# Kernel tuning notes

Measured on AMD Instinct MI355X. Metric: run time of the kernel, lower is better.

Reference implementation:

```python
import jax, jax.numpy as jnp
import numpy as np

EPS = 1e-9


def _pairwise_sqdist(x1, x2):
    # x1: (B,n,3), x2: (B,m,3) -> (B,n,m) squared euclidean distances
    s1 = jnp.sum(x1 * x1, axis=-1)
    s2 = jnp.sum(x2 * x2, axis=-1)
    cross = jnp.einsum('bnd,bmd->bnm', x1, x2)
    return jnp.maximum(s1[:, :, None] + s2[:, None, :] - 2.0 * cross, 0.0)


def _approxmatch(x1, x2):
    # Faithful port of the approxmatch CUDA kernel (Fan et al. EMD approx).
    B, n, _ = x1.shape
    m = x2.shape[1]
    if n >= m:
        multiL, multiR = 1.0, float(n // m)   # integer division as in CUDA
    else:
        multiL, multiR = float(m // n), 1.0
    dist = _pairwise_sqdist(x1, x2)  # (B,n,m)
    # j = 7 .. -1 -> level = -4^j ; j = -2 -> level = 0  (10 sweeps total)
    levels = jnp.concatenate([
        -(4.0 ** jnp.arange(7, -2, -1, dtype=jnp.float32)),
        jnp.zeros((1,), jnp.float32)])
    match0 = jnp.zeros((B, n, m), jnp.float32)
    remainL0 = jnp.full((B, n), multiL, jnp.float32)
    remainR0 = jnp.full((B, m), multiR, jnp.float32)

    def body(carry, level):
        match, remainL, remainR = carry
        e = jnp.exp(level * dist)                              # (B,n,m)
        suml = EPS + jnp.einsum('bnm,bm->bn', e, remainR)
        ratioL = remainL / suml                                # (B,n)
        sumr = remainR * jnp.einsum('bnm,bn->bm', e, ratioL)   # (B,m)
        consumption = jnp.minimum(remainR / (sumr + EPS), 1.0)
        ratioR = consumption * remainR                         # (B,m)
        remainR = jnp.maximum(0.0, remainR - sumr)
        w = e * ratioL[:, :, None] * ratioR[:, None, :]        # flow k->l
        match = match + w
        remainL = jnp.maximum(0.0, remainL - jnp.sum(w, axis=-1))
        return (match, remainL, remainR), None

    (match, _, _), _ = jax.lax.scan(body, (match0, remainL0, remainR0), levels)
    return match, dist


def setup_inputs() -> dict:
    key = jax.random.key(0)
    k1, k2 = jax.random.split(key)
    B, N = 4, 4096
    xyz1 = jax.random.normal(k1, (B, 3, N), dtype=jnp.float32)
    xyz2 = jax.random.normal(k2, (B, 3, N), dtype=jnp.float32)
    return {"xyz1": xyz1, "xyz2": xyz2}


def reference(xyz1, xyz2):
    # transpose=True: BCN -> BNC
    x1 = jnp.transpose(xyz1, (0, 2, 1))
    x2 = jnp.transpose(xyz2, (0, 2, 1))
    match, dist = _approxmatch(x1, x2)
    d = jnp.sqrt(jnp.maximum(dist, 1e-20))
    cost = jnp.sum(match * d, axis=(1, 2))            # (B,)
    emd = cost / min(x1.shape[1], x2.shape[1])
    return jnp.mean(emd)                               # reduce_mean=True
```

## Files before the change

kernel.cpp:

```cpp
#include <hip/hip_runtime.h>


#define NPTS 4096
#define BATCH 4
#define EMD_EPS 1e-9f
#define TILE 1024
#define RPW 2
#define THREADS 256
#define RPB 8
#define NBLK (NPTS / RPB)

typedef float v2f __attribute__((ext_vector_type(2)));

__device__ __forceinline__ float fexp2(float x) {
#if __has_builtin(__builtin_amdgcn_exp2f)
    return __builtin_amdgcn_exp2f(x);
#else
    return exp2f(x);
#endif
}
__device__ __forceinline__ float fsqrt(float x) {
#if __has_builtin(__builtin_amdgcn_sqrtf)
    return __builtin_amdgcn_sqrtf(x);
#else
    return __sqrtf(x);
#endif
}

__device__ __forceinline__ float wave_reduce(float v) {
    v += __shfl_xor(v, 32);
    v += __shfl_xor(v, 16);
    v += __shfl_xor(v, 8);
    v += __shfl_xor(v, 4);
    v += __shfl_xor(v, 2);
    v += __shfl_xor(v, 1);
    return v;
}

__global__ __launch_bounds__(THREADS, 6) void k_ratioL0(
        const float* __restrict__ xyz1, const float* __restrict__ xyz2,
        float* __restrict__ ratioL, float* __restrict__ remainL,
        float* __restrict__ remainR, float ls2) {
    const int b = blockIdx.y;
    const int tid = threadIdx.x;
    const int wave = tid >> 6;
    const int lane = tid & 63;
    const int row0 = blockIdx.x * RPB + wave * RPW;

    const float* x1 = xyz1 + b * 3 * NPTS;
    const float* x2 = xyz2 + b * 3 * NPTS;
    const float2* x2x = (const float2*)(x2);
    const float2* x2y = (const float2*)(x2 + NPTS);
    const float2* x2z = (const float2*)(x2 + 2 * NPTS);

    float px[RPW], py[RPW], pz[RPW];
    v2f acc[RPW];
#pragma unroll
    for (int r = 0; r < RPW; ++r) {
        px[r] = x1[row0 + r];
        py[r] = x1[NPTS + row0 + r];
        pz[r] = x1[2 * NPTS + row0 + r];
        acc[r] = (v2f)(0.0f);
    }
    __shared__ float4 sA[TILE / 2];
    __shared__ float2 sZ[TILE / 2];

    for (int c0 = 0; c0 < NPTS; c0 += TILE) {
        __syncthreads();
        for (int i = tid; i < TILE / 2; i += THREADS) {
            int e = c0 / 2 + i;
            float2 xx = x2x[e], yy = x2y[e];
            sA[i] = make_float4(xx.x, xx.y, yy.x, yy.y);
            sZ[i] = x2z[e];
        }
        __syncthreads();
#pragma unroll 2
        for (int j = 0; j < TILE / 128; ++j) {
            float4 a = sA[lane + 64 * j];
            float2 z = sZ[lane + 64 * j];
            v2f ax = {a.x, a.y}, ay = {a.z, a.w}, az = {z.x, z.y};
#pragma unroll
            for (int r = 0; r < RPW; ++r) {
                v2f dx = px[r] - ax, dy = py[r] - ay, dz = pz[r] - az;
                v2f d = dx * dx + dy * dy + dz * dz;
                v2f sd = ls2 * d;
                v2f e2 = {fexp2(sd.x), fexp2(sd.y)};
                acc[r] += e2;
            }
        }
    }
#pragma unroll
    for (int r = 0; r < RPW; ++r) {
        float s = wave_reduce(acc[r].x + acc[r].y);
        if (lane == 0) {
            int idx = b * NPTS + row0 + r;
            ratioL[idx] = 1.0f / (EMD_EPS + s);
            remainL[idx] = 1.0f;
            remainR[idx] = 1.0f;
        }
    }
}

__global__ __launch_bounds__(THREADS, 6) void k_ratioR(
        const float* __restrict__ xyz1, const float* __restrict__ xyz2,
        const float* __restrict__ ratioL, float* __restrict__ ratioR,
        float* __restrict__ remainR, float ls2) {
    const int b = blockIdx.y;
    const int tid = threadIdx.x;
    const int wave = tid >> 6;
    const int lane = tid & 63;
    const int col0 = blockIdx.x * RPB + wave * RPW;

    const float* x1 = xyz1 + b * 3 * NPTS;
    const float* x2 = xyz2 + b * 3 * NPTS;
    const float2* x1x = (const float2*)(x1);
    const float2* x1y = (const float2*)(x1 + NPTS);
    const float2* x1z = (const float2*)(x1 + 2 * NPTS);
    const float2* wLv = (const float2*)(ratioL + b * NPTS);

    float px[RPW], py[RPW], pz[RPW];
    v2f acc[RPW];
#pragma unroll
    for (int r = 0; r < RPW; ++r) {
        px[r] = x2[col0 + r];
        py[r] = x2[NPTS + col0 + r];
        pz[r] = x2[2 * NPTS + col0 + r];
        acc[r] = (v2f)(0.0f);
    }
    __shared__ float4 sA[TILE / 2];
    __shared__ float4 sB[TILE / 2];

    for (int c0 = 0; c0 < NPTS; c0 += TILE) {
        __syncthreads();
        for (int i = tid; i < TILE / 2; i += THREADS) {
            int e = c0 / 2 + i;
            float2 xx = x1x[e], yy = x1y[e], zz = x1z[e], ww = wLv[e];
            sA[i] = make_float4(xx.x, xx.y, yy.x, yy.y);
            sB[i] = make_float4(zz.x, zz.y, ww.x, ww.y);
        }
        __syncthreads();
#pragma unroll 2
        for (int j = 0; j < TILE / 128; ++j) {
            float4 a = sA[lane + 64 * j];
            float4 bq = sB[lane + 64 * j];
            v2f ax = {a.x, a.y}, ay = {a.z, a.w};
            v2f az = {bq.x, bq.y}, aw = {bq.z, bq.w};
#pragma unroll
            for (int r = 0; r < RPW; ++r) {
                v2f dx = px[r] - ax, dy = py[r] - ay, dz = pz[r] - az;
                v2f d = dx * dx + dy * dy + dz * dz;
                v2f sd = ls2 * d;
                v2f e2 = {fexp2(sd.x), fexp2(sd.y)};
                acc[r] += e2 * aw;
            }
        }
    }
#pragma unroll
    for (int r = 0; r < RPW; ++r) {
        float s = wave_reduce(acc[r].x + acc[r].y);
        if (lane == 0) {
            int idx = b * NPTS + col0 + r;
            float rv = remainR[idx];
            float sumr = rv * s;
            float cons = fminf(rv / (sumr + EMD_EPS), 1.0f);
            ratioR[idx] = cons * rv;
            remainR[idx] = fmaxf(0.0f, rv - sumr);
        }
    }
}

template <bool SQ>
__global__ __launch_bounds__(THREADS, 6) void k_cost_fused(
        const float* __restrict__ xyz1, const float* __restrict__ xyz2,
        float* __restrict__ ratioL, const float* __restrict__ ratioR,
        float* __restrict__ remainL, const float* __restrict__ remainR,
        float* __restrict__ cost_part, float ls2, float ls2n, int initCost) {
    const int b = blockIdx.y;
    const int tid = threadIdx.x;
    const int wave = tid >> 6;
    const int lane = tid & 63;
    const int row0 = blockIdx.x * RPB + wave * RPW;

    const float* x1 = xyz1 + b * 3 * NPTS;
    const float* x2 = xyz2 + b * 3 * NPTS;
    const float2* x2x = (const float2*)(x2);
    const float2* x2y = (const float2*)(x2 + NPTS);
    const float2* x2z = (const float2*)(x2 + 2 * NPTS);
    const float2* wRv = (const float2*)(ratioR + b * NPTS);
    const float2* w2v = (const float2*)(remainR + b * NPTS);

    float px[RPW], py[RPW], pz[RPW];
    v2f acc_a[RPW], acc_c[RPW], acc_s[RPW];
#pragma unroll
    for (int r = 0; r < RPW; ++r) {
        px[r] = x1[row0 + r];
        py[r] = x1[NPTS + row0 + r];
        pz[r] = x1[2 * NPTS + row0 + r];
        acc_a[r] = (v2f)(0.0f);
        acc_c[r] = (v2f)(0.0f);
        acc_s[r] = (v2f)(0.0f);
    }
    __shared__ float4 sA[TILE / 2];
    __shared__ float4 sB[TILE / 2];
    __shared__ float2 sC[TILE / 2];
    __shared__ float s_cost[THREADS / 64];

    for (int c0 = 0; c0 < NPTS; c0 += TILE) {
        __syncthreads();
        for (int i = tid; i < TILE / 2; i += THREADS) {
            int e = c0 / 2 + i;
            float2 xx = x2x[e], yy = x2y[e], zz = x2z[e], wr = wRv[e];
            sA[i] = make_float4(xx.x, xx.y, yy.x, yy.y);
            sB[i] = make_float4(zz.x, zz.y, wr.x, wr.y);
            sC[i] = w2v[e];
        }
        __syncthreads();
#pragma unroll 2
        for (int j = 0; j < TILE / 128; ++j) {
            float4 a = sA[lane + 64 * j];
            float4 bq = sB[lane + 64 * j];
            float2 c = sC[lane + 64 * j];
            v2f ax = {a.x, a.y}, ay = {a.z, a.w};
            v2f az = {bq.x, bq.y}, wr = {bq.z, bq.w};
            v2f cw = {c.x, c.y};
#pragma unroll
            for (int r = 0; r < RPW; ++r) {
                v2f dx = px[r] - ax, dy = py[r] - ay, dz = pz[r] - az;
                v2f d = dx * dx + dy * dy + dz * dz;
                v2f er;
                if (SQ) {
                    v2f sd = ls2n * d;
                    v2f e2 = {fexp2(sd.x), fexp2(sd.y)};
                    acc_s[r] += e2 * cw;
                    v2f e4 = e2 * e2;
                    er = (e4 * e4) * wr;
                } else {
                    v2f sd = ls2 * d;
                    v2f e1 = {fexp2(sd.x), fexp2(sd.y)};
                    er = e1 * wr;
                    acc_s[r] += cw;
                }
                acc_a[r] += er;
                v2f sq = {fsqrt(d.x), fsqrt(d.y)};
                acc_c[r] += er * sq;
            }
        }
    }
    float wcost = 0.0f;
#pragma unroll
    for (int r = 0; r < RPW; ++r) {
        float sa = wave_reduce(acc_a[r].x + acc_a[r].y);
        float sc = wave_reduce(acc_c[r].x + acc_c[r].y);
        float ss = wave_reduce(acc_s[r].x + acc_s[r].y);
        if (lane == 0) {
            int idx = b * NPTS + row0 + r;
            float rl = ratioL[idx];
            float rem = fmaxf(0.0f, remainL[idx] - rl * sa);
            remainL[idx] = rem;
            ratioL[idx] = rem / (EMD_EPS + ss);
            wcost = fmaf(rl, sc, wcost);
        }
    }
    if (lane == 0) s_cost[wave] = wcost;
    __syncthreads();
    if (tid == 0) {
        float t = s_cost[0] + s_cost[1] + s_cost[2] + s_cost[3];
        int ci = b * NBLK + blockIdx.x;
        cost_part[ci] = (initCost ? t : cost_part[ci] + t);
    }
}

__global__ void k_sum_ratioL(const float* __restrict__ ratioL, float* __restrict__ S_L) {
    const int b = blockIdx.x;
    const int tid = threadIdx.x;
    float s = 0.0f;
    for (int i = tid; i < NPTS; i += 256) s += ratioL[b * NPTS + i];
    s = wave_reduce(s);
    __shared__ float sw[4];
    if ((tid & 63) == 0) sw[tid >> 6] = s;
    __syncthreads();
    if (tid == 0) S_L[b] = sw[0] + sw[1] + sw[2] + sw[3];
}

__global__ __launch_bounds__(THREADS, 6) void k_cost_l0(
        const float* __restrict__ xyz1, const float* __restrict__ xyz2,
        const float* __restrict__ ratioL, const float* __restrict__ remainR,
        const float* __restrict__ S_L, float* __restrict__ cost_part) {
    const int b = blockIdx.y;
    const int tid = threadIdx.x;
    const int wave = tid >> 6;
    const int lane = tid & 63;
    const int row0 = blockIdx.x * RPB + wave * RPW;
    const float sL = S_L[b];

    const float* x1 = xyz1 + b * 3 * NPTS;
    const float* x2 = xyz2 + b * 3 * NPTS;
    const float2* x2x = (const float2*)(x2);
    const float2* x2y = (const float2*)(x2 + NPTS);
    const float2* x2z = (const float2*)(x2 + 2 * NPTS);
    const float2* wRv = (const float2*)(remainR + b * NPTS);

    float px[RPW], py[RPW], pz[RPW];
    v2f acc_c[RPW];
#pragma unroll
    for (int r = 0; r < RPW; ++r) {
        px[r] = x1[row0 + r];
        py[r] = x1[NPTS + row0 + r];
        pz[r] = x1[2 * NPTS + row0 + r];
        acc_c[r] = (v2f)(0.0f);
    }
    __shared__ float4 sA[TILE / 2];
    __shared__ float4 sB[TILE / 2];
    __shared__ float s_cost[THREADS / 64];

    for (int c0 = 0; c0 < NPTS; c0 += TILE) {
        __syncthreads();
        for (int i = tid; i < TILE / 2; i += THREADS) {
            int e = c0 / 2 + i;
            float2 xx = x2x[e], yy = x2y[e], zz = x2z[e], rv = wRv[e];
            float wr0 = fminf(rv.x / (rv.x * sL + EMD_EPS), 1.0f) * rv.x;
            float wr1 = fminf(rv.y / (rv.y * sL + EMD_EPS), 1.0f) * rv.y;
            sA[i] = make_float4(xx.x, xx.y, yy.x, yy.y);
            sB[i] = make_float4(zz.x, zz.y, wr0, wr1);
        }
        __syncthreads();
#pragma unroll 2
        for (int j = 0; j < TILE / 128; ++j) {
            float4 a = sA[lane + 64 * j];
            float4 bq = sB[lane + 64 * j];
            v2f ax = {a.x, a.y}, ay = {a.z, a.w};
            v2f az = {bq.x, bq.y}, wr = {bq.z, bq.w};
#pragma unroll
            for (int r = 0; r < RPW; ++r) {
                v2f dx = px[r] - ax, dy = py[r] - ay, dz = pz[r] - az;
                v2f d = dx * dx + dy * dy + dz * dz;
                v2f sq = {fsqrt(d.x), fsqrt(d.y)};
                acc_c[r] += wr * sq;
            }
        }
    }
    float wcost = 0.0f;
#pragma unroll
    for (int r = 0; r < RPW; ++r) {
        float sc = wave_reduce(acc_c[r].x + acc_c[r].y);
        if (lane == 0)
            wcost = fmaf(ratioL[b * NPTS + row0 + r], sc, wcost);
    }
    if (lane == 0) s_cost[wave] = wcost;
    __syncthreads();
    if (tid == 0) {
        float t = s_cost[0] + s_cost[1] + s_cost[2] + s_cost[3];
        cost_part[b * NBLK + blockIdx.x] += t;
    }
}

__global__ void k_final(const float* __restrict__ cost_part, float* __restrict__ out) {
    const int tid = threadIdx.x;
    float s = 0.0f;
    for (int i = tid; i < BATCH * NBLK; i += 256) s += cost_part[i];
    s = wave_reduce(s);
    __shared__ float sw[4];
    if ((tid & 63) == 0) sw[tid >> 6] = s;
    __syncthreads();
    if (tid == 0) out[0] = (sw[0] + sw[1] + sw[2] + sw[3]) / ((float)NPTS * (float)BATCH);
}

extern "C" void kernel_launch(void* const* d_in, const int* in_sizes, int n_in,
                              void* d_out, int out_size, void* d_ws, size_t ws_size,
                              hipStream_t stream) {
    const float* xyz1 = (const float*)d_in[0];
    const float* xyz2 = (const float*)d_in[1];
    float* out = (float*)d_out;

    const int BN = BATCH * NPTS;
    float* ws = (float*)d_ws;
    float* remainL  = ws;
    float* remainR  = ws + 1 * BN;
    float* ratioL   = ws + 2 * BN;
    float* ratioR   = ws + 3 * BN;
    float* cost_part = ws + 4 * BN;
    float* S_L      = cost_part + BATCH * NBLK;

    static const float levels[10] = {
        -16384.0f, -4096.0f, -1024.0f, -256.0f, -64.0f,
        -16.0f, -4.0f, -1.0f, -0.25f, 0.0f};
    float ls2[10];
    for (int t = 0; t < 10; ++t)
        ls2[t] = (float)(levels[t] * 1.4426950408889634);

    dim3 grid(NBLK, BATCH);

    k_ratioL0<<<grid, THREADS, 0, stream>>>(xyz1, xyz2, ratioL, remainL, remainR, ls2[0]);
    for (int t = 0; t < 8; ++t) {
        k_ratioR<<<grid, THREADS, 0, stream>>>(xyz1, xyz2, ratioL, ratioR, remainR, ls2[t]);
        k_cost_fused<true><<<grid, THREADS, 0, stream>>>(xyz1, xyz2, ratioL, ratioR,
                                                         remainL, remainR, cost_part,
                                                         ls2[t], ls2[t + 1], t == 0 ? 1 : 0);
    }
    k_ratioR<<<grid, THREADS, 0, stream>>>(xyz1, xyz2, ratioL, ratioR, remainR, ls2[8]);
    k_cost_fused<false><<<grid, THREADS, 0, stream>>>(xyz1, xyz2, ratioL, ratioR,
                                                      remainL, remainR, cost_part,
                                                      ls2[8], 0.0f, 0);
    k_sum_ratioL<<<BATCH, 256, 0, stream>>>(ratioL, S_L);
    k_cost_l0<<<grid, THREADS, 0, stream>>>(xyz1, xyz2, ratioL, remainR, S_L, cost_part);
    k_final<<<1, 256, 0, stream>>>(cost_part, out);
}
```

Baseline: 532.6 us.

## Sort points by x and skip far tiles using per-tile x bounds

Counting-sorts both point clouds by x coordinate and computes x min/max bounds for each 128-point tile. The inner loops of the ratioL, ratioR and cost kernels then skip a tile when its squared x-gap to the wave's rows makes the exponential underflow at that level. The cost kernel computes only the next-level sum when the current-level term is negligible, and the separate ratioL sum kernel is folded into an atomic add. This aims to cut the exp and sqrt work for the sharp early levels, at the cost of two extra kernels and wave-uniform branching. The skipped terms are approximations, but ones that underflow to near zero in float32.

```diff
diff --git a/kernel.cpp b/kernel.cpp
--- a/kernel.cpp
+++ b/kernel.cpp
@@ -9,6 +9,7 @@
 #define THREADS 256
 #define RPB 8
 #define NBLK (NPTS / RPB)
+#define NTILE 32
 
 typedef float v2f __attribute__((ext_vector_type(2)));
 
@@ -37,18 +38,98 @@
     return v;
 }
 
+__global__ __launch_bounds__(1024) void k_sortx(
+        const float* __restrict__ xyz1, const float* __restrict__ xyz2,
+        float* __restrict__ x1s, float* __restrict__ x2s) {
+    const int side = blockIdx.x, b = blockIdx.y;
+    const float* src = (side ? xyz2 : xyz1) + b * 3 * NPTS;
+    float* dst = (side ? x2s : x1s) + b * 3 * NPTS;
+    const int tid = threadIdx.x;
+    const int lane = tid & 63, wave = tid >> 6;
+
+    __shared__ unsigned hist[4096];
+    __shared__ unsigned short keys[4096];
+    __shared__ unsigned warr[16];
+
+    for (int i = tid; i < 4096; i += 1024) hist[i] = 0u;
+    __syncthreads();
+    for (int i = tid; i < NPTS; i += 1024) {
+        float x = src[i];
+        int k = (int)((x + 6.0f) * 341.0f);
+        k = min(max(k, 0), 4095);
+        keys[i] = (unsigned short)k;
+        atomicAdd(&hist[k], 1u);
+    }
+    __syncthreads();
+    const int base = tid * 4;
+    unsigned h0 = hist[base], h1 = hist[base + 1], h2 = hist[base + 2], h3 = hist[base + 3];
+    unsigned st = h0 + h1 + h2 + h3;
+    unsigned v = st;
+    for (int d = 1; d < 64; d <<= 1) {
+        unsigned u = __shfl_up(v, d);
+        if (lane >= d) v += u;
+    }
+    if (lane == 63) warr[wave] = v;
+    __syncthreads();
+    if (tid == 0) {
+        unsigned run = 0;
+        for (int w = 0; w < 16; ++w) { unsigned t = warr[w]; warr[w] = run; run += t; }
+    }
+    __syncthreads();
+    unsigned off = warr[wave] + (v - st);
+    hist[base] = off;
+    hist[base + 1] = off + h0;
+    hist[base + 2] = off + h0 + h1;
+    hist[base + 3] = off + h0 + h1 + h2;
+    __syncthreads();
+    for (int i = tid; i < NPTS; i += 1024) {
+        unsigned k = keys[i];
+        unsigned pos = atomicAdd(&hist[k], 1u);
+        dst[pos] = src[i];
+        dst[NPTS + pos] = src[NPTS + i];
+        dst[2 * NPTS + pos] = src[2 * NPTS + i];
+    }
+}
+
+__global__ void k_xbounds(const float* __restrict__ x1s, const float* __restrict__ x2s,
+                          float* __restrict__ bx1, float* __restrict__ bx2) {
+    const int tile = blockIdx.x, b = blockIdx.y, side = blockIdx.z;
+    const float* src = (side ? x2s : x1s) + b * 3 * NPTS + tile * 128;
+    float* o = (side ? bx2 : bx1) + (b * NTILE + tile) * 2;
+    const int lane = threadIdx.x;
+    float mn = 1e30f, mx = -1e30f;
+    for (int i = lane; i < 128; i += 64) {
+        float x = src[i];
+        mn = fminf(mn, x); mx = fmaxf(mx, x);
+    }
+    for (int d = 32; d; d >>= 1) {
+        mn = fminf(mn, __shfl_xor(mn, d));
+        mx = fmaxf(mx, __shfl_xor(mx, d));
+    }
+    if (lane == 0) { o[0] = mn; o[1] = mx; }
+}
+
+#define XMD2(ti)                                                             \
+    float bmn = sBB[(ti) * 2], bmx = sBB[(ti) * 2 + 1];                      \
+    float dd = fmaxf(0.0f, fmaxf(bmn - gmx, gmn - bmx));                     \
+    float md2 = dd * dd;
+
 __global__ __launch_bounds__(THREADS, 6) void k_ratioL0(
-        const float* __restrict__ xyz1, const float* __restrict__ xyz2,
+        const float* __restrict__ x1s, const float* __restrict__ x2s,
+        const float* __restrict__ bx2,
         float* __restrict__ ratioL, float* __restrict__ remainL,
-        float* __restrict__ remainR, float ls2) {
+        float* __restrict__ remainR, float* __restrict__ S_L,
+        float ls2, float thr) {
     const int b = blockIdx.y;
     const int tid = threadIdx.x;
     const int wave = tid >> 6;
     const int lane = tid & 63;
     const int row0 = blockIdx.x * RPB + wave * RPW;
 
-    const float* x1 = xyz1 + b * 3 * NPTS;
-    const float* x2 = xyz2 + b * 3 * NPTS;
+    if (blockIdx.x == 0 && tid == 0) S_L[b] = 0.0f;
+
+    const float* x1 = x1s + b * 3 * NPTS;
+    const float* x2 = x2s + b * 3 * NPTS;
     const float2* x2x = (const float2*)(x2);
     const float2* x2y = (const float2*)(x2 + NPTS);
     const float2* x2z = (const float2*)(x2 + 2 * NPTS);
@@ -62,8 +143,12 @@
         pz[r] = x1[2 * NPTS + row0 + r];
         acc[r] = (v2f)(0.0f);
     }
+    const float gmn = fminf(px[0], px[1]), gmx = fmaxf(px[0], px[1]);
+
     __shared__ float4 sA[TILE / 2];
     __shared__ float2 sZ[TILE / 2];
+    __shared__ float sBB[NTILE * 2];
+    if (tid < NTILE * 2) sBB[tid] = bx2[b * NTILE * 2 + tid];
 
     for (int c0 = 0; c0 < NPTS; c0 += TILE) {
         __syncthreads();
@@ -76,16 +161,19 @@
         __syncthreads();
 #pragma unroll 2
         for (int j = 0; j < TILE / 128; ++j) {
-            float4 a = sA[lane + 64 * j];
-            float2 z = sZ[lane + 64 * j];
-            v2f ax = {a.x, a.y}, ay = {a.z, a.w}, az = {z.x, z.y};
-#pragma unroll
-            for (int r = 0; r < RPW; ++r) {
-                v2f dx = px[r] - ax, dy = py[r] - ay, dz = pz[r] - az;
-                v2f d = dx * dx + dy * dy + dz * dz;
-                v2f sd = ls2 * d;
-                v2f e2 = {fexp2(sd.x), fexp2(sd.y)};
-                acc[r] += e2;
+            XMD2((c0 >> 7) + j);
+            if (md2 < thr) {
+                float4 a = sA[lane + 64 * j];
+                float2 z = sZ[lane + 64 * j];
+                v2f ax = {a.x, a.y}, ay = {a.z, a.w}, az = {z.x, z.y};
+#pragma unroll
+                for (int r = 0; r < RPW; ++r) {
+                    v2f dx = px[r] - ax, dy = py[r] - ay, dz = pz[r] - az;
+                    v2f d = dx * dx + dy * dy + dz * dz;
+                    v2f sd = ls2 * d;
+                    v2f e2 = {fexp2(sd.x), fexp2(sd.y)};
+                    acc[r] += e2;
+                }
             }
         }
     }
@@ -102,17 +190,18 @@
 }
 
 __global__ __launch_bounds__(THREADS, 6) void k_ratioR(
-        const float* __restrict__ xyz1, const float* __restrict__ xyz2,
+        const float* __restrict__ x1s, const float* __restrict__ x2s,
+        const float* __restrict__ bx1,
         const float* __restrict__ ratioL, float* __restrict__ ratioR,
-        float* __restrict__ remainR, float ls2) {
+        float* __restrict__ remainR, float ls2, float thr) {
     const int b = blockIdx.y;
     const int tid = threadIdx.x;
     const int wave = tid >> 6;
     const int lane = tid & 63;
     const int col0 = blockIdx.x * RPB + wave * RPW;
 
-    const float* x1 = xyz1 + b * 3 * NPTS;
-    const float* x2 = xyz2 + b * 3 * NPTS;
+    const float* x1 = x1s + b * 3 * NPTS;
+    const float* x2 = x2s + b * 3 * NPTS;
     const float2* x1x = (const float2*)(x1);
     const float2* x1y = (const float2*)(x1 + NPTS);
     const float2* x1z = (const float2*)(x1 + 2 * NPTS);
@@ -127,8 +216,12 @@
         pz[r] = x2[2 * NPTS + col0 + r];
         acc[r] = (v2f)(0.0f);
     }
+    const float gmn = fminf(px[0], px[1]), gmx = fmaxf(px[0], px[1]);
+
     __shared__ float4 sA[TILE / 2];
     __shared__ float4 sB[TILE / 2];
+    __shared__ float sBB[NTILE * 2];
+    if (tid < NTILE * 2) sBB[tid] = bx1[b * NTILE * 2 + tid];
 
     for (int c0 = 0; c0 < NPTS; c0 += TILE) {
         __syncthreads();
@@ -141,17 +234,20 @@
         __syncthreads();
 #pragma unroll 2
         for (int j = 0; j < TILE / 128; ++j) {
-            float4 a = sA[lane + 64 * j];
-            float4 bq = sB[lane + 64 * j];
-            v2f ax = {a.x, a.y}, ay = {a.z, a.w};
-            v2f az = {bq.x, bq.y}, aw = {bq.z, bq.w};
-#pragma unroll
-            for (int r = 0; r < RPW; ++r) {
-                v2f dx = px[r] - ax, dy = py[r] - ay, dz = pz[r] - az;
-                v2f d = dx * dx + dy * dy + dz * dz;
-                v2f sd = ls2 * d;
-                v2f e2 = {fexp2(sd.x), fexp2(sd.y)};
-                acc[r] += e2 * aw;
+            XMD2((c0 >> 7) + j);
+            if (md2 < thr) {
+                float4 a = sA[lane + 64 * j];
+                float4 bq = sB[lane + 64 * j];
+                v2f ax = {a.x, a.y}, ay = {a.z, a.w};
+                v2f az = {bq.x, bq.y}, aw = {bq.z, bq.w};
+#pragma unroll
+                for (int r = 0; r < RPW; ++r) {
+                    v2f dx = px[r] - ax, dy = py[r] - ay, dz = pz[r] - az;
+                    v2f d = dx * dx + dy * dy + dz * dz;
+                    v2f sd = ls2 * d;
+                    v2f e2 = {fexp2(sd.x), fexp2(sd.y)};
+                    acc[r] += e2 * aw;
+                }
             }
         }
     }
@@ -171,18 +267,21 @@
 
 template <bool SQ>
 __global__ __launch_bounds__(THREADS, 6) void k_cost_fused(
-        const float* __restrict__ xyz1, const float* __restrict__ xyz2,
+        const float* __restrict__ x1s, const float* __restrict__ x2s,
+        const float* __restrict__ bx2,
         float* __restrict__ ratioL, const float* __restrict__ ratioR,
         float* __restrict__ remainL, const float* __restrict__ remainR,
-        float* __restrict__ cost_part, float ls2, float ls2n, int initCost) {
+        float* __restrict__ S_L, float* __restrict__ cost_part,
+        float ls2, float ls2n, float thrF, float thrT,
+        int initCost, int addSL) {
     const int b = blockIdx.y;
     const int tid = threadIdx.x;
     const int wave = tid >> 6;
     const int lane = tid & 63;
     const int row0 = blockIdx.x * RPB + wave * RPW;
 
-    const float* x1 = xyz1 + b * 3 * NPTS;
-    const float* x2 = xyz2 + b * 3 * NPTS;
+    const float* x1 = x1s + b * 3 * NPTS;
+    const float* x2 = x2s + b * 3 * NPTS;
     const float2* x2x = (const float2*)(x2);
     const float2* x2y = (const float2*)(x2 + NPTS);
     const float2* x2z = (const float2*)(x2 + 2 * NPTS);
@@ -200,10 +299,14 @@
         acc_c[r] = (v2f)(0.0f);
         acc_s[r] = (v2f)(0.0f);
     }
+    const float gmn = fminf(px[0], px[1]), gmx = fmaxf(px[0], px[1]);
+
     __shared__ float4 sA[TILE / 2];
     __shared__ float4 sB[TILE / 2];
     __shared__ float2 sC[TILE / 2];
+    __shared__ float sBB[NTILE * 2];
     __shared__ float s_cost[THREADS / 64];
+    if (tid < NTILE * 2) sBB[tid] = bx2[b * NTILE * 2 + tid];
 
     for (int c0 = 0; c0 < NPTS; c0 += TILE) {
         __syncthreads();
@@ -217,32 +320,46 @@
         __syncthreads();
 #pragma unroll 2
         for (int j = 0; j < TILE / 128; ++j) {
-            float4 a = sA[lane + 64 * j];
-            float4 bq = sB[lane + 64 * j];
-            float2 c = sC[lane + 64 * j];
-            v2f ax = {a.x, a.y}, ay = {a.z, a.w};
-            v2f az = {bq.x, bq.y}, wr = {bq.z, bq.w};
-            v2f cw = {c.x, c.y};
-#pragma unroll
-            for (int r = 0; r < RPW; ++r) {
-                v2f dx = px[r] - ax, dy = py[r] - ay, dz = pz[r] - az;
-                v2f d = dx * dx + dy * dy + dz * dz;
-                v2f er;
-                if (SQ) {
-                    v2f sd = ls2n * d;
-                    v2f e2 = {fexp2(sd.x), fexp2(sd.y)};
-                    acc_s[r] += e2 * cw;
-                    v2f e4 = e2 * e2;
-                    er = (e4 * e4) * wr;
+            XMD2((c0 >> 7) + j);
+            if (md2 < thrF) {
+                float4 a = sA[lane + 64 * j];
+                float4 bq = sB[lane + 64 * j];
+                float2 c = sC[lane + 64 * j];
+                v2f ax = {a.x, a.y}, ay = {a.z, a.w};
+                v2f az = {bq.x, bq.y}, wr = {bq.z, bq.w};
+                v2f cw = {c.x, c.y};
+                if (SQ && md2 >= thrT) {
+#pragma unroll
+                    for (int r = 0; r < RPW; ++r) {
+                        v2f dx = px[r] - ax, dy = py[r] - ay, dz = pz[r] - az;
+                        v2f d = dx * dx + dy * dy + dz * dz;
+                        v2f sd = ls2n * d;
+                        v2f e2 = {fexp2(sd.x), fexp2(sd.y)};
+                        acc_s[r] += e2 * cw;
+                    }
                 } else {
-                    v2f sd = ls2 * d;
-                    v2f e1 = {fexp2(sd.x), fexp2(sd.y)};
-                    er = e1 * wr;
-                    acc_s[r] += cw;
+#pragma unroll
+                    for (int r = 0; r < RPW; ++r) {
+                        v2f dx = px[r] - ax, dy = py[r] - ay, dz = pz[r] - az;
+                        v2f d = dx * dx + dy * dy + dz * dz;
+                        v2f er;
+                        if (SQ) {
+                            v2f sd = ls2n * d;
+                            v2f e2 = {fexp2(sd.x), fexp2(sd.y)};
+                            acc_s[r] += e2 * cw;
+                            v2f e4 = e2 * e2;
+                            er = (e4 * e4) * wr;
+                        } else {
+                            v2f sd = ls2 * d;
+                            v2f e1 = {fexp2(sd.x), fexp2(sd.y)};
+                            er = e1 * wr;
+                            acc_s[r] += cw;
+                        }
+                        acc_a[r] += er;
+                        v2f sq = {fsqrt(d.x), fsqrt(d.y)};
+                        acc_c[r] += er * sq;
+                    }
                 }
-                acc_a[r] += er;
-                v2f sq = {fsqrt(d.x), fsqrt(d.y)};
-                acc_c[r] += er * sq;
             }
         }
     }
@@ -257,7 +374,9 @@
             float rl = ratioL[idx];
             float rem = fmaxf(0.0f, remainL[idx] - rl * sa);
             remainL[idx] = rem;
-            ratioL[idx] = rem / (EMD_EPS + ss);
+            float nrl = rem / (EMD_EPS + ss);
+            ratioL[idx] = nrl;
+            if (addSL) atomicAdd(&S_L[b], nrl);
             wcost = fmaf(rl, sc, wcost);
         }
     }
@@ -270,20 +389,8 @@
     }
 }
 
-__global__ void k_sum_ratioL(const float* __restrict__ ratioL, float* __restrict__ S_L) {
-    const int b = blockIdx.x;
-    const int tid = threadIdx.x;
-    float s = 0.0f;
-    for (int i = tid; i < NPTS; i += 256) s += ratioL[b * NPTS + i];
-    s = wave_reduce(s);
-    __shared__ float sw[4];
-    if ((tid & 63) == 0) sw[tid >> 6] = s;
-    __syncthreads();
-    if (tid == 0) S_L[b] = sw[0] + sw[1] + sw[2] + sw[3];
-}
-
 __global__ __launch_bounds__(THREADS, 6) void k_cost_l0(
-        const float* __restrict__ xyz1, const float* __restrict__ xyz2,
+        const float* __restrict__ x1s, const float* __restrict__ x2s,
         const float* __restrict__ ratioL, const float* __restrict__ remainR,
         const float* __restrict__ S_L, float* __restrict__ cost_part) {
     const int b = blockIdx.y;
@@ -293,8 +400,8 @@
     const int row0 = blockIdx.x * RPB + wave * RPW;
     const float sL = S_L[b];
 
-    const float* x1 = xyz1 + b * 3 * NPTS;
-    const float* x2 = xyz2 + b * 3 * NPTS;
+    const float* x1 = x1s + b * 3 * NPTS;
+    const float* x2 = x2s + b * 3 * NPTS;
     const float2* x2x = (const float2*)(x2);
     const float2* x2y = (const float2*)(x2 + NPTS);
     const float2* x2z = (const float2*)(x2 + 2 * NPTS);
@@ -374,34 +481,46 @@
 
     const int BN = BATCH * NPTS;
     float* ws = (float*)d_ws;
-    float* remainL  = ws;
-    float* remainR  = ws + 1 * BN;
-    float* ratioL   = ws + 2 * BN;
-    float* ratioR   = ws + 3 * BN;
+    float* remainL   = ws;
+    float* remainR   = ws + 1 * BN;
+    float* ratioL    = ws + 2 * BN;
+    float* ratioR    = ws + 3 * BN;
     float* cost_part = ws + 4 * BN;
-    float* S_L      = cost_part + BATCH * NBLK;
+    float* S_L       = cost_part + BATCH * NBLK;
+    float* x1s       = S_L + 4;
+    float* x2s       = x1s + 3 * BN;
+    float* bx1       = x2s + 3 * BN;
+    float* bx2       = bx1 + BATCH * NTILE * 2;
 
     static const float levels[10] = {
         -16384.0f, -4096.0f, -1024.0f, -256.0f, -64.0f,
         -16.0f, -4.0f, -1.0f, -0.25f, 0.0f};
-    float ls2[10];
-    for (int t = 0; t < 10; ++t)
+    float ls2[10], thrR[10];
+    for (int t = 0; t < 10; ++t) {
         ls2[t] = (float)(levels[t] * 1.4426950408889634);
+        thrR[t] = (t < 9) ? (168.0f / -ls2[t]) : 3.0e38f;
+    }
+    const float INF_THR = 3.0e38f;
 
     dim3 grid(NBLK, BATCH);
 
-    k_ratioL0<<<grid, THREADS, 0, stream>>>(xyz1, xyz2, ratioL, remainL, remainR, ls2[0]);
+    k_sortx<<<dim3(2, BATCH), 1024, 0, stream>>>(xyz1, xyz2, x1s, x2s);
+    k_xbounds<<<dim3(NTILE, BATCH, 2), 64, 0, stream>>>(x1s, x2s, bx1, bx2);
+
+    k_ratioL0<<<grid, THREADS, 0, stream>>>(x1s, x2s, bx2, ratioL, remainL, remainR,
+                                            S_L, ls2[0], thrR[0]);
     for (int t = 0; t < 8; ++t) {
-        k_ratioR<<<grid, THREADS, 0, stream>>>(xyz1, xyz2, ratioL, ratioR, remainR, ls2[t]);
-        k_cost_fused<true><<<grid, THREADS, 0, stream>>>(xyz1, xyz2, ratioL, ratioR,
-                                                         remainL, remainR, cost_part,
-                                                         ls2[t], ls2[t + 1], t == 0 ? 1 : 0);
-    }
-    k_ratioR<<<grid, THREADS, 0, stream>>>(xyz1, xyz2, ratioL, ratioR, remainR, ls2[8]);
-    k_cost_fused<false><<<grid, THREADS, 0, stream>>>(xyz1, xyz2, ratioL, ratioR,
-                                                      remainL, remainR, cost_part,
-                                                      ls2[8], 0.0f, 0);
-    k_sum_ratioL<<<BATCH, 256, 0, stream>>>(ratioL, S_L);
-    k_cost_l0<<<grid, THREADS, 0, stream>>>(xyz1, xyz2, ratioL, remainR, S_L, cost_part);
+        k_ratioR<<<grid, THREADS, 0, stream>>>(x1s, x2s, bx1, ratioL, ratioR, remainR,
+                                               ls2[t], thrR[t]);
+        k_cost_fused<true><<<grid, THREADS, 0, stream>>>(
+            x1s, x2s, bx2, ratioL, ratioR, remainL, remainR, S_L, cost_part,
+            ls2[t], ls2[t + 1], 4.0f * thrR[t], thrR[t], t == 0 ? 1 : 0, 0);
+    }
+    k_ratioR<<<grid, THREADS, 0, stream>>>(x1s, x2s, bx1, ratioL, ratioR, remainR,
+                                           ls2[8], thrR[8]);
+    k_cost_fused<false><<<grid, THREADS, 0, stream>>>(
+        x1s, x2s, bx2, ratioL, ratioR, remainL, remainR, S_L, cost_part,
+        ls2[8], 0.0f, INF_THR, INF_THR, 0, 1);
+    k_cost_l0<<<grid, THREADS, 0, stream>>>(x1s, x2s, ratioL, remainR, S_L, cost_part);
     k_final<<<1, 256, 0, stream>>>(cost_part, out);
 }
```

New measurement: 700.5 us. 1.32x slower.
